# Optimization experiments

Measured on AMD Instinct MI355X. Metric: run time of the kernel, lower is better.

Reference implementation:

```python
import jax, jax.numpy as jnp
import numpy as np

D_MODEL = 512
N_HEADS = 8
HEAD_DIM = D_MODEL // N_HEADS
BATCH = 4
SEQ = 2048


def setup_inputs() -> dict:
    key = jax.random.key(0)
    ks = jax.random.split(key, 9)
    s = 1.0 / np.sqrt(D_MODEL)
    inp = {
        "x": jax.random.normal(ks[0], (BATCH, SEQ, D_MODEL), dtype=jnp.float32),
        "wq": jax.random.uniform(ks[1], (D_MODEL, D_MODEL), jnp.float32, -s, s),
        "bq": jax.random.uniform(ks[2], (D_MODEL,), jnp.float32, -s, s),
        "wk": jax.random.uniform(ks[3], (D_MODEL, D_MODEL), jnp.float32, -s, s),
        "bk": jax.random.uniform(ks[4], (D_MODEL,), jnp.float32, -s, s),
        "wv": jax.random.uniform(ks[5], (D_MODEL, D_MODEL), jnp.float32, -s, s),
        "bv": jax.random.uniform(ks[6], (D_MODEL,), jnp.float32, -s, s),
        "wo": jax.random.uniform(ks[7], (D_MODEL, D_MODEL), jnp.float32, -s, s),
        "bo": jax.random.uniform(ks[8], (D_MODEL,), jnp.float32, -s, s),
    }
    return inp


def reference(x, wq, bq, wk, bk, wv, bv, wo, bo):
    B, S, D = x.shape
    H, Hd = N_HEADS, HEAD_DIM
    # projections (torch Linear: y = x @ W^T + b; here weights stored as [in, out])
    q = (x @ wq + bq).reshape(B, S, H, Hd).transpose(0, 2, 1, 3)  # [B,H,S,Hd]
    k = (x @ wk + bk).reshape(B, S, H, Hd).transpose(0, 2, 1, 3)
    v = (x @ wv + bv).reshape(B, S, H, Hd).transpose(0, 2, 1, 3)
    scores = jnp.einsum("bhqd,bhkd->bhqk", q, k) / jnp.sqrt(jnp.float32(Hd))
    attn = jax.nn.softmax(scores, axis=-1)
    o = jnp.einsum("bhqk,bhkd->bhqd", attn, v)  # [B,H,S,Hd]
    o = o.transpose(0, 2, 1, 3).reshape(B, S, D)
    return o @ wo + bo
```

## Files before the change

kernel.cpp:

```cpp
#include <hip/hip_runtime.h>
#include <math.h>

#define DM   512
#define SEQL 2048
#define NB   4
#define NH   8
#define HD   64

typedef _Float16 f16;
typedef __fp16   fp16x2 __attribute__((ext_vector_type(2)));
typedef _Float16 f16x4 __attribute__((ext_vector_type(4)));
typedef _Float16 f16x8 __attribute__((ext_vector_type(8)));
typedef float    f32x4 __attribute__((ext_vector_type(4)));

#define QSCALE 0.1803368801f
#define SOFTMAX_SHIFT 4.328085123f
#define PSTR 88

typedef const __attribute__((address_space(1))) void* gp1_t;
typedef __attribute__((address_space(3))) void* lp3_t;
__device__ __forceinline__ void glds16(const void* g, void* l) {
    __builtin_amdgcn_global_load_lds((gp1_t)g, (lp3_t)l, 16, 0, 0);
}

__device__ __forceinline__ float fast_exp2(float x) {
    return __builtin_amdgcn_exp2f(x);
}

__global__ __launch_bounds__(256) void prep_kernel(
    const float* __restrict__ x, f16* __restrict__ xh,
    const float* __restrict__ w0, const float* __restrict__ w1,
    const float* __restrict__ w2, const float* __restrict__ w3,
    f16* __restrict__ o0, f16* __restrict__ o1,
    f16* __restrict__ o2, f16* __restrict__ o3)
{
    __shared__ f16 t[64][72];
    const int bx = blockIdx.x;
    if (bx < 2048) {
        int i = (bx * 256 + threadIdx.x) * 8;
        float4 a = *(const float4*)&x[i];
        float4 b = *(const float4*)&x[i + 4];
        f16x8 h;
        h[0] = (f16)a.x; h[1] = (f16)a.y; h[2] = (f16)a.z; h[3] = (f16)a.w;
        h[4] = (f16)b.x; h[5] = (f16)b.y; h[6] = (f16)b.z; h[7] = (f16)b.w;
        *(f16x8*)&xh[i] = h;
        return;
    }
    const int idx  = bx - 2048;
    const int wsel = idx >> 6, tile = idx & 63;
    const float* w; f16* o;
    switch (wsel) {
        case 0:  w = w0; o = o0; break;
        case 1:  w = w1; o = o1; break;
        case 2:  w = w2; o = o2; break;
        default: w = w3; o = o3; break;
    }
    const int n0 = (tile & 7) * 64, k0 = (tile >> 3) * 64;
    const int tx = threadIdx.x & 63, tg = threadIdx.x >> 6;
    #pragma unroll
    for (int r = 0; r < 16; ++r) {
        int kl = tg * 16 + r;
        t[tx][kl] = (f16)w[(size_t)(k0 + kl) * DM + n0 + tx];
    }
    __syncthreads();
    #pragma unroll
    for (int r = 0; r < 16; ++r) {
        int nl = tg * 16 + r;
        o[(size_t)(n0 + nl) * DM + k0 + tx] = t[nl][tx];
    }
}

__global__ __launch_bounds__(256) void gemm_qkv(
    const f16* __restrict__ A, const f16* __restrict__ Wt,
    const float* __restrict__ bq, const float* __restrict__ bk,
    const float* __restrict__ bv,
    f16* __restrict__ qh, f16* __restrict__ kh, f16* __restrict__ vth)
{
    __shared__ __align__(16) char smem[34816];
    f16* As_ = (f16*)smem;
    f16* Bs_ = (f16*)(smem + 16384);
    f16* T   = (f16*)smem;

    const int tid  = threadIdx.x;
    const int lane = tid & 63, wave = tid >> 6;
    const int quad = lane >> 4, l15 = lane & 15;
    const int wm = wave >> 1, wn = wave & 1;

    const int bid = blockIdx.x;
    const int r8  = bid & 7;
    const int tt  = bid >> 3;
    const int j   = tt % 12;
    const int mm  = tt / 12;
    const int n0  = j * 128;
    const int m0  = (mm * 8 + r8) * 128;
    const bool qk = (j < 8);

    const int sr16 = lane >> 2;
    const int sk   = (lane & 3) * 8;

    f32x4 acc[4][4] = {};

    for (int k0 = 0; k0 < DM; k0 += 64) {
        #pragma unroll
        for (int kh2 = 0; kh2 < 2; ++kh2) {
            #pragma unroll
            for (int rb = 0; rb < 2; ++rb) {
                const int row = wave * 32 + rb * 16;
                glds16(&A [(size_t)(m0 + row + sr16) * DM + k0 + kh2 * 32 + sk],
                       &As_[kh2 * 4096 + row * 32]);
                glds16(&Wt[(size_t)(n0 + row + sr16) * DM + k0 + kh2 * 32 + sk],
                       &Bs_[kh2 * 4096 + row * 32]);
            }
        }
        __syncthreads();

        #pragma unroll
        for (int kh2 = 0; kh2 < 2; ++kh2) {
            f16x8 af[4], bf[4];
            #pragma unroll
            for (int i = 0; i < 4; ++i)
                af[i] = *(f16x8*)&As_[kh2 * 4096 + (wm * 64 + i * 16 + l15) * 32 + quad * 8];
            #pragma unroll
            for (int i = 0; i < 4; ++i)
                bf[i] = *(f16x8*)&Bs_[kh2 * 4096 + (wn * 64 + i * 16 + l15) * 32 + quad * 8];
            if (qk) {
                #pragma unroll
                for (int i = 0; i < 4; ++i)
                    #pragma unroll
                    for (int jj = 0; jj < 4; ++jj)
                        acc[i][jj] = __builtin_amdgcn_mfma_f32_16x16x32_f16(
                            bf[i], af[jj], acc[i][jj], 0, 0, 0);
            } else {
                #pragma unroll
                for (int i = 0; i < 4; ++i)
                    #pragma unroll
                    for (int jj = 0; jj < 4; ++jj)
                        acc[i][jj] = __builtin_amdgcn_mfma_f32_16x16x32_f16(
                            af[i], bf[jj], acc[i][jj], 0, 0, 0);
            }
        }
        __syncthreads();
    }

    const int seg  = n0 >> 9;
    const int nn0b = n0 & 511;
    const int b    = m0 >> 11, s0 = m0 & 2047;

    if (qk) {
        const float* bp = seg == 0 ? bq : bk;
        #pragma unroll
        for (int i = 0; i < 4; ++i) {
            const int nb = wn * 64 + i * 16 + quad * 4;
            f32x4 bv4 = *(const f32x4*)&bp[nn0b + nb];
            #pragma unroll
            for (int jj = 0; jj < 4; ++jj) {
                const int ml = wm * 64 + jj * 16 + l15;
                f16x4 pk;
                #pragma unroll
                for (int rr = 0; rr < 4; ++rr) pk[rr] = (f16)(acc[i][jj][rr] + bv4[rr]);
                *(f16x4*)&T[ml * 136 + nb] = pk;
            }
        }
        __syncthreads();
        f16* op = seg == 0 ? qh : kh;
        #pragma unroll
        for (int r = 0; r < 8; ++r) {
            const int idx = r * 256 + tid;
            const int ml = idx >> 4, c = (idx & 15) * 8;
            f16x8 v = *(f16x8*)&T[ml * 136 + c];
            const int nn = nn0b + c;
            const int hh = nn >> 6, hd8 = nn & 63;
            *(f16x8*)&op[(((size_t)(b * NH + hh) * SEQL + s0 + ml) << 6) + hd8] = v;
        }
    } else {
        #pragma unroll
        for (int jj = 0; jj < 4; ++jj) {
            const int nl = wn * 64 + jj * 16 + l15;
            const float bias = bv[nn0b + nl];
            #pragma unroll
            for (int i = 0; i < 4; ++i) {
                const int mb = wm * 64 + i * 16 + quad * 4;
                f16x4 pk;
                #pragma unroll
                for (int rr = 0; rr < 4; ++rr) pk[rr] = (f16)(acc[i][jj][rr] + bias);
                *(f16x4*)&T[nl * 136 + mb] = pk;
            }
        }
        __syncthreads();
        #pragma unroll
        for (int r = 0; r < 8; ++r) {
            const int idx = r * 256 + tid;
            const int nl = idx >> 4, c = (idx & 15) * 8;
            f16x8 v = *(f16x8*)&T[nl * 136 + c];
            const int nn = nn0b + nl;
            const int hh = nn >> 6, hd = nn & 63;
            *(f16x8*)&vth[(((size_t)(b * NH + hh) * HD + hd) << 11) + s0 + c] = v;
        }
    }
}

__global__ __launch_bounds__(256) void gemm_out(
    const f16* __restrict__ A, const f16* __restrict__ Wt,
    const float* __restrict__ bias, float* __restrict__ out)
{
    __shared__ __align__(16) char smem[33792];
    f16*   As_ = (f16*)smem;
    f16*   Bs_ = (f16*)(smem + 8192);
    float* T3  = (float*)smem;

    const int tid  = threadIdx.x;
    const int lane = tid & 63, wave = tid >> 6;
    const int quad = lane >> 4, l15 = lane & 15;
    const int wn = wave >> 1, wm = wave & 1;
    const int n0 = blockIdx.x * 128, m0 = blockIdx.y * 64;

    const int sr16 = lane >> 2;
    const int sk   = (lane & 3) * 8;

    f32x4 acc[4][2] = {};

    for (int k0 = 0; k0 < DM; k0 += 64) {
        #pragma unroll
        for (int kh2 = 0; kh2 < 2; ++kh2) {
            {
                const int row = wave * 16;
                glds16(&A[(size_t)(m0 + row + sr16) * DM + k0 + kh2 * 32 + sk],
                       &As_[kh2 * 2048 + row * 32]);
            }
            #pragma unroll
            for (int rb = 0; rb < 2; ++rb) {
                const int row = wave * 32 + rb * 16;
                glds16(&Wt[(size_t)(n0 + row + sr16) * DM + k0 + kh2 * 32 + sk],
                       &Bs_[kh2 * 4096 + row * 32]);
            }
        }
        __syncthreads();

        #pragma unroll
        for (int kh2 = 0; kh2 < 2; ++kh2) {
            f16x8 af[4], bf[2];
            #pragma unroll
            for (int i = 0; i < 4; ++i)
                af[i] = *(f16x8*)&Bs_[kh2 * 4096 + (wn * 64 + i * 16 + l15) * 32 + quad * 8];
            #pragma unroll
            for (int jj = 0; jj < 2; ++jj)
                bf[jj] = *(f16x8*)&As_[kh2 * 2048 + (wm * 32 + jj * 16 + l15) * 32 + quad * 8];
            #pragma unroll
            for (int i = 0; i < 4; ++i)
                #pragma unroll
                for (int jj = 0; jj < 2; ++jj)
                    acc[i][jj] = __builtin_amdgcn_mfma_f32_16x16x32_f16(
                        af[i], bf[jj], acc[i][jj], 0, 0, 0);
        }
        __syncthreads();
    }

    #pragma unroll
    for (int i = 0; i < 4; ++i) {
        const int nb = wn * 64 + i * 16 + quad * 4;
        f32x4 bv4 = *(const f32x4*)&bias[n0 + nb];
        #pragma unroll
        for (int jj = 0; jj < 2; ++jj) {
            const int ml = wm * 32 + jj * 16 + l15;
            *(f32x4*)&T3[ml * 132 + nb] = acc[i][jj] + bv4;
        }
    }
    __syncthreads();
    #pragma unroll
    for (int r = 0; r < 8; ++r) {
        const int idx = r * 256 + tid;
        const int ml = idx >> 5, c = (idx & 31) * 4;
        f32x4 v = *(f32x4*)&T3[ml * 132 + c];
        *(f32x4*)&out[(size_t)(m0 + ml) * DM + n0 + c] = v;
    }
}

__global__ __launch_bounds__(512) void flash_attn_mfma(
    const f16* __restrict__ Q, const f16* __restrict__ K,
    const f16* __restrict__ Vt, f16* __restrict__ O)
{
    __shared__ __align__(16) char smem[80896];
    f16*   Ks = (f16*)smem;
    f16*   Vs = (f16*)(smem + 18432);
    f16*   Ps = (f16*)(smem + 35840);
    float* cs = (float*)smem;
    float* Lx = (float*)(smem + 34816);

    const int tid  = threadIdx.x;
    const int lane = tid & 63, wave = tid >> 6;
    const int quad = lane >> 4, l15 = lane & 15;
    const int g  = wave >> 2;
    const int qg = wave & 3;

    const int id = blockIdx.x;
    const int r8 = id & 7;
    const int tt = id >> 3;
    const int j  = tt & 15;
    const int bh = (tt >> 4) * 8 + r8;
    const int q0 = j * 128;
    const int b = bh >> 3, h = bh & 7;
    f16* Pw = Ps + wave * (32 * PSTR);

    const f16* Qb = Q  + (size_t)bh * SEQL * HD;
    const f16* Kb = K  + (size_t)bh * SEQL * HD;
    const f16* Vb = Vt + (size_t)bh * HD * SEQL;

    f16x8 qf[2][2];
    #pragma unroll
    for (int mq = 0; mq < 2; ++mq)
        #pragma unroll
        for (int ks = 0; ks < 2; ++ks) {
            qf[mq][ks] = *(const f16x8*)
                &Qb[(size_t)(q0 + qg * 32 + mq * 16 + l15) * HD + ks * 32 + quad * 8];
            #pragma unroll
            for (int jj = 0; jj < 8; ++jj) qf[mq][ks][jj] *= (f16)QSCALE;
        }

    f16x8 onesf;
    #pragma unroll
    for (int jj = 0; jj < 8; ++jj) onesf[jj] = (f16)1.0f;

    const int krow = tid >> 3, kch = (tid & 7) * 8;
    const int vrow = tid >> 4, vch = (tid & 15) * 8;

    f16x8 kreg[2], vreg[2];
    #pragma unroll
    for (int r = 0; r < 2; ++r) {
        kreg[r] = *(const f16x8*)&Kb[(size_t)(krow + r * 64) * HD + kch];
        vreg[r] = *(const f16x8*)&Vb[(size_t)(vrow + r * 32) * SEQL + vch];
    }

    f32x4 o_acc[2][4] = {};
    f32x4 o_l[2] = {};

    for (int kt = 0; kt < SEQL / 128; ++kt) {
        __syncthreads();
        #pragma unroll
        for (int r = 0; r < 2; ++r) {
            *(f16x8*)&Ks[(krow + r * 64) * 72 + kch]  = kreg[r];
            *(f16x8*)&Vs[(vrow + r * 32) * 136 + vch] = vreg[r];
        }
        __syncthreads();
        if (kt < SEQL / 128 - 1) {
            const int kb2 = (kt + 1) * 128;
            #pragma unroll
            for (int r = 0; r < 2; ++r) {
                kreg[r] = *(const f16x8*)&Kb[(size_t)(kb2 + krow + r * 64) * HD + kch];
                vreg[r] = *(const f16x8*)&Vb[(size_t)(vrow + r * 32) * SEQL + kb2 + vch];
            }
        }

        f32x4 sc[4][2];
        #pragma unroll
        for (int mk = 0; mk < 4; ++mk)
            #pragma unroll
            for (int mq = 0; mq < 2; ++mq)
                sc[mk][mq] = (f32x4){-SOFTMAX_SHIFT, -SOFTMAX_SHIFT,
                                     -SOFTMAX_SHIFT, -SOFTMAX_SHIFT};
        #pragma unroll
        for (int ks = 0; ks < 2; ++ks) {
            #pragma unroll
            for (int mk = 0; mk < 4; ++mk) {
                f16x8 af = *(f16x8*)&Ks[(g * 64 + mk * 16 + l15) * 72 + ks * 32 + quad * 8];
                #pragma unroll
                for (int mq = 0; mq < 2; ++mq)
                    sc[mk][mq] = __builtin_amdgcn_mfma_f32_16x16x32_f16(
                        af, qf[mq][ks], sc[mk][mq], 0, 0, 0);
            }
        }

        #pragma unroll
        for (int mk = 0; mk < 4; ++mk)
            #pragma unroll
            for (int mq = 0; mq < 2; ++mq) {
                float p0 = fast_exp2(sc[mk][mq][0]);
                float p1 = fast_exp2(sc[mk][mq][1]);
                float p2 = fast_exp2(sc[mk][mq][2]);
                float p3 = fast_exp2(sc[mk][mq][3]);
                union { f16x4 v4; fp16x2 v2[2]; } pk;
                pk.v2[0] = __builtin_amdgcn_cvt_pkrtz(p0, p1);
                pk.v2[1] = __builtin_amdgcn_cvt_pkrtz(p2, p3);
                *(f16x4*)&Pw[(mq * 16 + l15) * PSTR + mk * 16 + quad * 4] = pk.v4;
            }

        #pragma unroll
        for (int kc = 0; kc < 2; ++kc) {
            f16x8 pa0 = *(f16x8*)&Pw[(l15)      * PSTR + kc * 32 + quad * 8];
            f16x8 pa1 = *(f16x8*)&Pw[(16 + l15) * PSTR + kc * 32 + quad * 8];
            o_l[0] = __builtin_amdgcn_mfma_f32_16x16x32_f16(pa0, onesf, o_l[0], 0, 0, 0);
            o_l[1] = __builtin_amdgcn_mfma_f32_16x16x32_f16(pa1, onesf, o_l[1], 0, 0, 0);
            #pragma unroll
            for (int nt = 0; nt < 4; ++nt) {
                f16x8 vb = *(f16x8*)&Vs[(nt * 16 + l15) * 136 + g * 64 + kc * 32 + quad * 8];
                o_acc[0][nt] = __builtin_amdgcn_mfma_f32_16x16x32_f16(
                    pa0, vb, o_acc[0][nt], 0, 0, 0);
                o_acc[1][nt] = __builtin_amdgcn_mfma_f32_16x16x32_f16(
                    pa1, vb, o_acc[1][nt], 0, 0, 0);
            }
        }
    }

    __syncthreads();
    if (l15 == 0) {
        #pragma unroll
        for (int mq = 0; mq < 2; ++mq)
            #pragma unroll
            for (int r = 0; r < 4; ++r)
                Lx[wave * 32 + mq * 16 + quad * 4 + r] = o_l[mq][r];
    }
    if (g == 1) {
        #pragma unroll
        for (int mq = 0; mq < 2; ++mq)
            #pragma unroll
            for (int r = 0; r < 4; ++r) {
                const int ql = mq * 16 + quad * 4 + r;
                #pragma unroll
                for (int nt = 0; nt < 4; ++nt)
                    cs[(qg * 32 + ql) * 68 + nt * 16 + l15] = o_acc[mq][nt][r];
            }
    }
    __syncthreads();
    if (g == 0) {
        #pragma unroll
        for (int mq = 0; mq < 2; ++mq)
            #pragma unroll
            for (int r = 0; r < 4; ++r) {
                const int ql = mq * 16 + quad * 4 + r;
                const float inv = 1.0f / (Lx[qg * 32 + ql] + Lx[(4 + qg) * 32 + ql]);
                const int s = q0 + qg * 32 + ql;
                #pragma unroll
                for (int nt = 0; nt < 4; ++nt) {
                    float ov = o_acc[mq][nt][r] + cs[(qg * 32 + ql) * 68 + nt * 16 + l15];
                    O[((size_t)(b * SEQL + s)) * DM + h * HD + nt * 16 + l15] =
                        (f16)(ov * inv);
                }
            }
    }
}

extern "C" void kernel_launch(void* const* d_in, const int* in_sizes, int n_in,
                              void* d_out, int out_size, void* d_ws, size_t ws_size,
                              hipStream_t stream) {
    const float* x  = (const float*)d_in[0];
    const float* wq = (const float*)d_in[1];
    const float* bq = (const float*)d_in[2];
    const float* wk = (const float*)d_in[3];
    const float* bk = (const float*)d_in[4];
    const float* wv = (const float*)d_in[5];
    const float* bv = (const float*)d_in[6];
    const float* wo = (const float*)d_in[7];
    const float* bo = (const float*)d_in[8];

    const size_t NE = (size_t)NB * SEQL * DM;
    const size_t WE = (size_t)DM * DM;
    f16* xh    = (f16*)d_ws;
    f16* wqkvt = xh + NE;
    f16* wot   = wqkvt + 3 * WE;
    f16* qh    = wot + WE;
    f16* kh    = qh + NE;
    f16* vth   = kh + NE;
    f16* oh    = vth + NE;

    prep_kernel<<<2304, 256, 0, stream>>>(
        x, xh, wq, wk, wv, wo,
        wqkvt, wqkvt + WE, wqkvt + 2 * WE, wot);

    gemm_qkv<<<768, 256, 0, stream>>>(
        xh, wqkvt, bq, bk, bv, qh, kh, vth);

    flash_attn_mfma<<<512, 512, 0, stream>>>(qh, kh, vth, oh);

    gemm_out<<<dim3(4, 128), 256, 0, stream>>>(oh, wot, bo, (float*)d_out);
}
```

Baseline: 171.5 us.

## Double-buffer GEMM K-loop staging and split attention launch in two halves

```diff
diff --git a/kernel.cpp b/kernel.cpp
--- a/kernel.cpp
+++ b/kernel.cpp
@@ -98,49 +98,49 @@
     const int sr16 = lane >> 2;
     const int sk   = (lane & 3) * 8;
 
+    auto stage = [&](int k0, int buf) {
+        #pragma unroll
+        for (int rb = 0; rb < 2; ++rb) {
+            const int row = wave * 32 + rb * 16;
+            glds16(&A [(size_t)(m0 + row + sr16) * DM + k0 + sk],
+                   &As_[buf * 4096 + row * 32]);
+            glds16(&Wt[(size_t)(n0 + row + sr16) * DM + k0 + sk],
+                   &Bs_[buf * 4096 + row * 32]);
+        }
+    };
+
     f32x4 acc[4][4] = {};
-
-    for (int k0 = 0; k0 < DM; k0 += 64) {
-        #pragma unroll
-        for (int kh2 = 0; kh2 < 2; ++kh2) {
-            #pragma unroll
-            for (int rb = 0; rb < 2; ++rb) {
-                const int row = wave * 32 + rb * 16;
-                glds16(&A [(size_t)(m0 + row + sr16) * DM + k0 + kh2 * 32 + sk],
-                       &As_[kh2 * 4096 + row * 32]);
-                glds16(&Wt[(size_t)(n0 + row + sr16) * DM + k0 + kh2 * 32 + sk],
-                       &Bs_[kh2 * 4096 + row * 32]);
-            }
-        }
-        __syncthreads();
-
-        #pragma unroll
-        for (int kh2 = 0; kh2 < 2; ++kh2) {
-            f16x8 af[4], bf[4];
+    stage(0, 0);
+
+    for (int it = 0; it < 16; ++it) {
+        __syncthreads();
+        if (it < 15) stage((it + 1) * 32, (it + 1) & 1);
+        const int buf = (it & 1) * 4096;
+
+        f16x8 af[4], bf[4];
+        #pragma unroll
+        for (int i = 0; i < 4; ++i)
+            af[i] = *(f16x8*)&As_[buf + (wm * 64 + i * 16 + l15) * 32 + quad * 8];
+        #pragma unroll
+        for (int i = 0; i < 4; ++i)
+            bf[i] = *(f16x8*)&Bs_[buf + (wn * 64 + i * 16 + l15) * 32 + quad * 8];
+        if (qk) {
             #pragma unroll
             for (int i = 0; i < 4; ++i)
-                af[i] = *(f16x8*)&As_[kh2 * 4096 + (wm * 64 + i * 16 + l15) * 32 + quad * 8];
+                #pragma unroll
+                for (int jj = 0; jj < 4; ++jj)
+                    acc[i][jj] = __builtin_amdgcn_mfma_f32_16x16x32_f16(
+                        bf[i], af[jj], acc[i][jj], 0, 0, 0);
+        } else {
             #pragma unroll
             for (int i = 0; i < 4; ++i)
-                bf[i] = *(f16x8*)&Bs_[kh2 * 4096 + (wn * 64 + i * 16 + l15) * 32 + quad * 8];
-            if (qk) {
-                #pragma unroll
-                for (int i = 0; i < 4; ++i)
-                    #pragma unroll
-                    for (int jj = 0; jj < 4; ++jj)
-                        acc[i][jj] = __builtin_amdgcn_mfma_f32_16x16x32_f16(
-                            bf[i], af[jj], acc[i][jj], 0, 0, 0);
-            } else {
-                #pragma unroll
-                for (int i = 0; i < 4; ++i)
-                    #pragma unroll
-                    for (int jj = 0; jj < 4; ++jj)
-                        acc[i][jj] = __builtin_amdgcn_mfma_f32_16x16x32_f16(
-                            af[i], bf[jj], acc[i][jj], 0, 0, 0);
-            }
-        }
-        __syncthreads();
-    }
+                #pragma unroll
+                for (int jj = 0; jj < 4; ++jj)
+                    acc[i][jj] = __builtin_amdgcn_mfma_f32_16x16x32_f16(
+                        af[i], bf[jj], acc[i][jj], 0, 0, 0);
+        }
+    }
+    __syncthreads();
 
     const int seg  = n0 >> 9;
     const int nn0b = n0 & 511;
@@ -217,43 +217,41 @@
     const int sr16 = lane >> 2;
     const int sk   = (lane & 3) * 8;
 
+    auto stage = [&](int k0, int buf) {
+        const int rowA = wave * 16;
+        glds16(&A[(size_t)(m0 + rowA + sr16) * DM + k0 + sk],
+               &As_[buf * 2048 + rowA * 32]);
+        #pragma unroll
+        for (int rb = 0; rb < 2; ++rb) {
+            const int rowB = wave * 32 + rb * 16;
+            glds16(&Wt[(size_t)(n0 + rowB + sr16) * DM + k0 + sk],
+                   &Bs_[buf * 4096 + rowB * 32]);
+        }
+    };
+
     f32x4 acc[4][2] = {};
-
-    for (int k0 = 0; k0 < DM; k0 += 64) {
-        #pragma unroll
-        for (int kh2 = 0; kh2 < 2; ++kh2) {
-            {
-                const int row = wave * 16;
-                glds16(&A[(size_t)(m0 + row + sr16) * DM + k0 + kh2 * 32 + sk],
-                       &As_[kh2 * 2048 + row * 32]);
-            }
-            #pragma unroll
-            for (int rb = 0; rb < 2; ++rb) {
-                const int row = wave * 32 + rb * 16;
-                glds16(&Wt[(size_t)(n0 + row + sr16) * DM + k0 + kh2 * 32 + sk],
-                       &Bs_[kh2 * 4096 + row * 32]);
-            }
-        }
-        __syncthreads();
-
-        #pragma unroll
-        for (int kh2 = 0; kh2 < 2; ++kh2) {
-            f16x8 af[4], bf[2];
-            #pragma unroll
-            for (int i = 0; i < 4; ++i)
-                af[i] = *(f16x8*)&Bs_[kh2 * 4096 + (wn * 64 + i * 16 + l15) * 32 + quad * 8];
+    stage(0, 0);
+
+    for (int it = 0; it < 16; ++it) {
+        __syncthreads();
+        if (it < 15) stage((it + 1) * 32, (it + 1) & 1);
+        const int bufA = (it & 1) * 2048, bufB = (it & 1) * 4096;
+
+        f16x8 af[4], bf[2];
+        #pragma unroll
+        for (int i = 0; i < 4; ++i)
+            af[i] = *(f16x8*)&Bs_[bufB + (wn * 64 + i * 16 + l15) * 32 + quad * 8];
+        #pragma unroll
+        for (int jj = 0; jj < 2; ++jj)
+            bf[jj] = *(f16x8*)&As_[bufA + (wm * 32 + jj * 16 + l15) * 32 + quad * 8];
+        #pragma unroll
+        for (int i = 0; i < 4; ++i)
             #pragma unroll
             for (int jj = 0; jj < 2; ++jj)
-                bf[jj] = *(f16x8*)&As_[kh2 * 2048 + (wm * 32 + jj * 16 + l15) * 32 + quad * 8];
-            #pragma unroll
-            for (int i = 0; i < 4; ++i)
-                #pragma unroll
-                for (int jj = 0; jj < 2; ++jj)
-                    acc[i][jj] = __builtin_amdgcn_mfma_f32_16x16x32_f16(
-                        af[i], bf[jj], acc[i][jj], 0, 0, 0);
-        }
-        __syncthreads();
-    }
+                acc[i][jj] = __builtin_amdgcn_mfma_f32_16x16x32_f16(
+                    af[i], bf[jj], acc[i][jj], 0, 0, 0);
+    }
+    __syncthreads();
 
     #pragma unroll
     for (int i = 0; i < 4; ++i) {
@@ -277,7 +275,7 @@
 
 __global__ __launch_bounds__(512) void flash_attn_mfma(
     const f16* __restrict__ Q, const f16* __restrict__ K,
-    const f16* __restrict__ Vt, f16* __restrict__ O)
+    const f16* __restrict__ Vt, f16* __restrict__ O, int base)
 {
     __shared__ __align__(16) char smem[80896];
     f16*   Ks = (f16*)smem;
@@ -292,7 +290,7 @@
     const int g  = wave >> 2;
     const int qg = wave & 3;
 
-    const int id = blockIdx.x;
+    const int id = blockIdx.x + base;
     const int r8 = id & 7;
     const int tt = id >> 3;
     const int j  = tt & 15;
@@ -468,7 +466,8 @@
     gemm_qkv<<<768, 256, 0, stream>>>(
         xh, wqkvt, bq, bk, bv, qh, kh, vth);
 
-    flash_attn_mfma<<<512, 512, 0, stream>>>(qh, kh, vth, oh);
+    flash_attn_mfma<<<256, 512, 0, stream>>>(qh, kh, vth, oh, 0);
+    flash_attn_mfma<<<256, 512, 0, stream>>>(qh, kh, vth, oh, 256);
 
     gemm_out<<<dim3(4, 128), 256, 0, stream>>>(oh, wot, bo, (float*)d_out);
 }
```

New measurement: 173.3 us. Within noise of the previous version (+1.0%).
